# Optimization experiments

Hardware: AMD Instinct MI355X
Metric: run time of the kernel (lower is better)

Reference implementation:

```python
import jax, jax.numpy as jnp
import numpy as np

B, L, E, H = 2, 2048, 1024, 16
D = E // H
EPS = 1e-5


def setup_inputs() -> dict:
    key = jax.random.key(0)
    ks = jax.random.split(key, 12)
    s = 1.0 / np.sqrt(E)
    x = jax.random.normal(ks[0], (B, L, E), dtype=jnp.float32)
    # bool mask: True = block. Causal upper-triangular mask (L, S) with S == L.
    mask = jnp.triu(jnp.ones((L, L), dtype=jnp.bool_), k=1)
    Wq = jax.random.normal(ks[1], (E, E), jnp.float32) * s
    bq = jax.random.normal(ks[2], (E,), jnp.float32) * 0.01
    Wk = jax.random.normal(ks[3], (E, E), jnp.float32) * s
    bk = jax.random.normal(ks[4], (E,), jnp.float32) * 0.01
    Wv = jax.random.normal(ks[5], (E, E), jnp.float32) * s
    bv = jax.random.normal(ks[6], (E,), jnp.float32) * 0.01
    Wo = jax.random.normal(ks[7], (E, E), jnp.float32) * s
    bo = jax.random.normal(ks[8], (E,), jnp.float32) * 0.01
    gamma = jnp.ones((E,), jnp.float32)
    beta = jnp.zeros((E,), jnp.float32)
    return {"x": x, "mask": mask, "Wq": Wq, "bq": bq, "Wk": Wk, "bk": bk,
            "Wv": Wv, "bv": bv, "Wo": Wo, "bo": bo, "gamma": gamma, "beta": beta}


def reference(x, mask, Wq, bq, Wk, bk, Wv, bv, Wo, bo, gamma, beta):
    b, l, e = x.shape
    x = jnp.nan_to_num(x, nan=0.0, posinf=1e9, neginf=-1e9)
    # QKV projections (torch Linear: x @ W.T + b), split heads -> (B,H,L,D)
    q = (x @ Wq.T + bq).reshape(b, l, H, D).transpose(0, 2, 1, 3)
    k = (x @ Wk.T + bk).reshape(b, l, H, D).transpose(0, 2, 1, 3)
    v = (x @ Wv.T + bv).reshape(b, l, H, D).transpose(0, 2, 1, 3)
    scale = max(D ** 0.5, 1e-6)
    scores = jnp.einsum('bhtd,bhsd->bhts', q, k) / scale  # (B,H,L,L)
    # bool mask True=block -> additive -inf, broadcast (L,L) over (B,H)
    scores = scores + jnp.where(mask, -jnp.inf, 0.0).astype(scores.dtype)
    scores = scores - jnp.max(scores, axis=-1, keepdims=True)
    scores = jnp.nan_to_num(scores, nan=0.0, posinf=1e9, neginf=-1e9)
    attn = jax.nn.softmax(scores, axis=-1)
    o = jnp.einsum('bhts,bhsd->bhtd', attn, v)
    o = o.transpose(0, 2, 1, 3).reshape(b, l, e)
    y = o @ Wo.T + bo
    r = y + x
    # LayerNorm over last dim
    mu = jnp.mean(r, axis=-1, keepdims=True)
    var = jnp.mean((r - mu) ** 2, axis=-1, keepdims=True)
    out = (r - mu) * jax.lax.rsqrt(var + EPS) * gamma + beta
    out = jnp.nan_to_num(out, nan=0.0, posinf=1e9, neginf=-1e9)
    return out
```

## Files before the change

kernel.cpp:

```cpp
#include <hip/hip_runtime.h>
#include <hip/hip_bf16.h>
#include <cstdint>
#include <cstddef>

#define NB 2
#define NL 2048
#define NE 1024
#define NH 16
#define ND 64
#define NM (NB * NL)

typedef float f32x4 __attribute__((ext_vector_type(4)));
typedef __bf16 bf16x8 __attribute__((ext_vector_type(8)));
typedef __bf16 bf16x4 __attribute__((ext_vector_type(4)));

#define DEV static __device__ __forceinline__

DEV f32x4 mfma16(bf16x8 a, bf16x8 b, f32x4 c) {
  return __builtin_amdgcn_mfma_f32_16x16x32_bf16(a, b, c, 0, 0, 0);
}

DEV ushort f2bf(float f) {
  uint32_t u = __float_as_uint(f);
  uint32_t r = (u + 0x7fffu + ((u >> 16) & 1u)) >> 16;
  return (ushort)r;
}

#if __has_builtin(__builtin_amdgcn_exp2f)
DEV float fast_exp2(float x) { return __builtin_amdgcn_exp2f(x); }
#else
DEV float fast_exp2(float x) { return exp2f(x); }
#endif

DEV void gl_lds16(const void* src, void* lds_dst) {
  __builtin_amdgcn_global_load_lds(
      (const __attribute__((address_space(1))) void*)src,
      (__attribute__((address_space(3))) void*)lds_dst, 16, 0, 0);
}

template <int NCALLS>
DEV void stage_swz(const char* gbase, size_t row_stride_b, char* lds_base, int tid) {
#pragma unroll
  for (int c = 0; c < NCALLS; ++c) {
    uint32_t P = (uint32_t)(c * 4096 + tid * 16);
    uint32_t r = P >> 7;
    uint32_t Lo = P ^ ((r & 7u) << 4);
    gl_lds16(gbase + (size_t)r * row_stride_b + (Lo & 127u), lds_base + P);
  }
}

__global__ __launch_bounds__(256) void pack_kernel(
    const float* __restrict__ x, const float* __restrict__ wq,
    const float* __restrict__ wk, const float* __restrict__ wv,
    const float* __restrict__ wo, ushort* __restrict__ xb,
    ushort* __restrict__ wqb, ushort* __restrict__ wkb,
    ushort* __restrict__ wvb, ushort* __restrict__ wob) {
  int64_t q = (int64_t)blockIdx.x * 256 + threadIdx.x;
  const float* src;
  ushort* dst;
  bool cl;
  if (q < 1048576) {
    src = x + q * 4;
    dst = xb + q * 4;
    cl = true;
  } else {
    int64_t r = q - 1048576;
    int wsel = (int)(r >> 18);
    int64_t o = (r & 262143) * 4;
    cl = false;
    if (wsel == 0) { src = wq + o; dst = wqb + o; }
    else if (wsel == 1) { src = wk + o; dst = wkb + o; }
    else if (wsel == 2) { src = wv + o; dst = wvb + o; }
    else { src = wo + o; dst = wob + o; }
  }
  float4 v = *(const float4*)src;
  if (cl) {
    v.x = (v.x != v.x) ? 0.f : fminf(fmaxf(v.x, -1e9f), 1e9f);
    v.y = (v.y != v.y) ? 0.f : fminf(fmaxf(v.y, -1e9f), 1e9f);
    v.z = (v.z != v.z) ? 0.f : fminf(fmaxf(v.z, -1e9f), 1e9f);
    v.w = (v.w != v.w) ? 0.f : fminf(fmaxf(v.w, -1e9f), 1e9f);
  }
  ushort4 o4;
  o4.x = f2bf(v.x);
  o4.y = f2bf(v.y);
  o4.z = f2bf(v.z);
  o4.w = f2bf(v.w);
  *(ushort4*)dst = o4;
}

__global__ __launch_bounds__(256) void qkv_gemm_kernel(
    const ushort* __restrict__ xb, const ushort* __restrict__ wqb,
    const ushort* __restrict__ wkb, const ushort* __restrict__ wvb,
    const float* __restrict__ bq, const float* __restrict__ bk,
    const float* __restrict__ bv, ushort* __restrict__ Qo,
    ushort* __restrict__ Ko, ushort* __restrict__ Vto) {
  __shared__ __align__(128) char lds[65536];
  const int tid = threadIdx.x;
  const int w = tid >> 6, ln = tid & 63;
  const int ln15 = ln & 15, g = ln >> 4;
  const int wm = w >> 1, wn = w & 1;
  const int m0 = blockIdx.y * 128;
  const int which = blockIdx.x >> 3;
  const int n0w = (blockIdx.x & 7) * 128;
  const ushort* Wb = (which == 0) ? wqb : (which == 1) ? wkb : wvb;

  const char* Abase = (const char*)xb + (size_t)m0 * 2048;
  const char* Bbase = (const char*)Wb + (size_t)n0w * 2048;

  f32x4 acc[4][4];
#pragma unroll
  for (int m = 0; m < 4; ++m)
#pragma unroll
    for (int n = 0; n < 4; ++n) acc[m][n] = {0.f, 0.f, 0.f, 0.f};

  int cur = 0;
  stage_swz<4>(Abase, 2048, lds, tid);
  stage_swz<4>(Bbase, 2048, lds + 32768, tid);

  for (int kt = 0; kt < 16; ++kt) {
    if (kt + 1 < 16) {
      stage_swz<4>(Abase + (kt + 1) * 128, 2048, lds + (cur ^ 1) * 16384, tid);
      stage_swz<4>(Bbase + (kt + 1) * 128, 2048,
                   lds + 32768 + (cur ^ 1) * 16384, tid);
      asm volatile("s_waitcnt vmcnt(8)" ::: "memory");
    } else {
      asm volatile("s_waitcnt vmcnt(0)" ::: "memory");
    }
    __builtin_amdgcn_s_barrier();
    asm volatile("" ::: "memory");
    const char* ab = lds + cur * 16384;
    const char* bb = lds + 32768 + cur * 16384;
    __builtin_amdgcn_s_setprio(1);
#pragma unroll
    for (int kc = 0; kc < 2; ++kc) {
      bf16x8 af[4], bfr[4];
#pragma unroll
      for (int i = 0; i < 4; ++i) {
        uint32_t ar = (uint32_t)(wm * 64 + i * 16 + ln15);
        uint32_t ao = (ar * 128u + (uint32_t)(kc * 64 + g * 16)) ^ ((ar & 7u) << 4);
        af[i] = *(const bf16x8*)(ab + ao);
        uint32_t br = (uint32_t)(wn * 64 + i * 16 + ln15);
        uint32_t bo_ = (br * 128u + (uint32_t)(kc * 64 + g * 16)) ^ ((br & 7u) << 4);
        bfr[i] = *(const bf16x8*)(bb + bo_);
      }
#pragma unroll
      for (int m = 0; m < 4; ++m)
#pragma unroll
        for (int n = 0; n < 4; ++n) acc[m][n] = mfma16(af[m], bfr[n], acc[m][n]);
    }
    __builtin_amdgcn_s_setprio(0);
    asm volatile("s_waitcnt lgkmcnt(0)" ::: "memory");
    __builtin_amdgcn_s_barrier();
    asm volatile("" ::: "memory");
    cur ^= 1;
  }

  const float* bias = (which == 0) ? bq : (which == 1) ? bk : bv;
  const float sc = (which == 0) ? 0.18033688011112042f : 1.0f;
#pragma unroll
  for (int n = 0; n < 4; ++n) {
    const int col = n0w + wn * 64 + n * 16 + ln15;
    const int h = col >> 6, d = col & 63;
    const float bc = bias[col];
#pragma unroll
    for (int m = 0; m < 4; ++m) {
      if (which < 2) {
        ushort* dst = (which == 0) ? Qo : Ko;
#pragma unroll
        for (int j = 0; j < 4; ++j) {
          int mg = m0 + wm * 64 + m * 16 + g * 4 + j;
          int b = mg >> 11, l = mg & 2047;
          dst[((size_t)(b * NH + h) * NL + l) * ND + d] = f2bf((acc[m][n][j] + bc) * sc);
        }
      } else {
        int mg0 = m0 + wm * 64 + m * 16 + g * 4;
        int b = mg0 >> 11, l0 = mg0 & 2047;
        ushort4 pk;
        pk.x = f2bf(acc[m][n][0] + bc);
        pk.y = f2bf(acc[m][n][1] + bc);
        pk.z = f2bf(acc[m][n][2] + bc);
        pk.w = f2bf(acc[m][n][3] + bc);
        *(ushort4*)(Vto + ((size_t)(b * NH + h) * ND + d) * NL + l0) = pk;
      }
    }
  }
}

__global__ __launch_bounds__(256) void attn_kernel(
    const ushort* __restrict__ Q, const ushort* __restrict__ K,
    const ushort* __restrict__ Vt, ushort* __restrict__ Op) {
  __shared__ __align__(128) char lds[40960];
  const int tid = threadIdx.x;
  const int w = tid >> 6, ln = tid & 63;
  const int ln15 = ln & 15, g = ln >> 4;
  const int bx = blockIdx.x;
  const int kk = (bx >> 5) & 7, bsel = bx >> 8, bh = bx & 31;
  const int qt = (bsel == 0) ? 31 - kk : (bsel == 1) ? kk
               : (bsel == 2) ? 23 - kk : 8 + kk;
  const int b = bh >> 4, h = bh & 15;
  const ushort* Qh = Q + (size_t)bh * NL * ND;
  const ushort* Kh = K + (size_t)bh * NL * ND;
  const ushort* Vth = Vt + (size_t)bh * ND * NL;
  const uint32_t pbase = 32768u + (uint32_t)w * 2048u;

  const int qb = qt * 64;
  const int r0 = qb + w * 16;
  const int nt = qt + 1;

  bf16x8 qf[2];
#pragma unroll
  for (int kc = 0; kc < 2; ++kc)
    qf[kc] = *(const bf16x8*)(Qh + (size_t)(r0 + ln15) * ND + kc * 32 + g * 8);

  f32x4 o_acc[4];
#pragma unroll
  for (int n = 0; n < 4; ++n) o_acc[n] = {0.f, 0.f, 0.f, 0.f};
  float m_run = -1e30f, l_run = 0.f;

  int cur = 0;
  stage_swz<2>((const char*)Kh, 128, lds, tid);
  stage_swz<2>((const char*)Vth, (size_t)NL * 2, lds + 16384, tid);

  for (int t = 0; t < nt; ++t) {
    const int s0 = t * 64;
    if (t + 1 < nt) {
      stage_swz<2>((const char*)Kh + (size_t)(s0 + 64) * 128, 128,
                   lds + (cur ^ 1) * 8192, tid);
      stage_swz<2>((const char*)Vth + (size_t)(s0 + 64) * 2, (size_t)NL * 2,
                   lds + 16384 + (cur ^ 1) * 8192, tid);
      asm volatile("s_waitcnt vmcnt(4)" ::: "memory");
    } else {
      asm volatile("s_waitcnt vmcnt(0)" ::: "memory");
    }
    __builtin_amdgcn_s_barrier();
    asm volatile("" ::: "memory");

    const char* kb = lds + cur * 8192;
    const char* vb = lds + 16384 + cur * 8192;

    f32x4 s_acc[4];
#pragma unroll
    for (int n = 0; n < 4; ++n) s_acc[n] = {0.f, 0.f, 0.f, 0.f};
    __builtin_amdgcn_s_setprio(1);
#pragma unroll
    for (int kc = 0; kc < 2; ++kc) {
      bf16x8 kf[4];
#pragma unroll
      for (int n = 0; n < 4; ++n) {
        uint32_t kr = (uint32_t)(n * 16 + ln15);
        uint32_t off = (kr * 128u + (uint32_t)(kc * 64 + g * 16)) ^ ((kr & 7u) << 4);
        kf[n] = *(const bf16x8*)(kb + off);
      }
#pragma unroll
      for (int n = 0; n < 4; ++n) s_acc[n] = mfma16(kf[n], qf[kc], s_acc[n]);
    }
    __builtin_amdgcn_s_setprio(0);

    if (t == nt - 1) {
      const int qi = r0 + ln15;
#pragma unroll
      for (int n = 0; n < 4; ++n)
#pragma unroll
        for (int j = 0; j < 4; ++j) {
          int si = s0 + n * 16 + g * 4 + j;
          s_acc[n][j] = (si > qi) ? -1e30f : s_acc[n][j];
        }
    }

    float mx = s_acc[0][0];
#pragma unroll
    for (int n = 0; n < 4; ++n)
#pragma unroll
      for (int j = 0; j < 4; ++j) mx = fmaxf(mx, s_acc[n][j]);
    mx = fmaxf(mx, __shfl_xor(mx, 16));
    mx = fmaxf(mx, __shfl_xor(mx, 32));
    if (__any(mx > m_run + 8.0f)) {
      float mn = fmaxf(m_run, mx);
      float al = fast_exp2(m_run - mn);
      m_run = mn;
      l_run *= al;
#pragma unroll
      for (int j = 0; j < 4; ++j) {
        float aj = __shfl(al, g * 4 + j);
#pragma unroll
        for (int n = 0; n < 4; ++n) o_acc[n][j] *= aj;
      }
    }
    float ps = 0.f;
#pragma unroll
    for (int n = 0; n < 4; ++n) {
      float p0 = fast_exp2(s_acc[n][0] - m_run);
      float p1 = fast_exp2(s_acc[n][1] - m_run);
      float p2 = fast_exp2(s_acc[n][2] - m_run);
      float p3 = fast_exp2(s_acc[n][3] - m_run);
      ps += (p0 + p1) + (p2 + p3);
      bf16x4 pk = {(__bf16)p0, (__bf16)p1, (__bf16)p2, (__bf16)p3};
      uint32_t off = ((uint32_t)ln15 * 128u + (uint32_t)(n * 32 + g * 8)) ^
                     (((uint32_t)ln15 & 7u) << 4);
      *(bf16x4*)(lds + pbase + off) = pk;
    }
    ps += __shfl_xor(ps, 16);
    ps += __shfl_xor(ps, 32);
    l_run += ps;

    __builtin_amdgcn_s_setprio(1);
#pragma unroll
    for (int kc = 0; kc < 2; ++kc) {
      uint32_t poff = ((uint32_t)ln15 * 128u + (uint32_t)(kc * 64 + g * 16)) ^
                      (((uint32_t)ln15 & 7u) << 4);
      bf16x8 pf = *(const bf16x8*)(lds + pbase + poff);
      bf16x8 vf[4];
#pragma unroll
      for (int n = 0; n < 4; ++n) {
        uint32_t vr = (uint32_t)(n * 16 + ln15);
        uint32_t off = (vr * 128u + (uint32_t)(kc * 64 + g * 16)) ^ ((vr & 7u) << 4);
        vf[n] = *(const bf16x8*)(vb + off);
      }
#pragma unroll
      for (int n = 0; n < 4; ++n) o_acc[n] = mfma16(pf, vf[n], o_acc[n]);
    }
    __builtin_amdgcn_s_setprio(0);

    asm volatile("s_waitcnt lgkmcnt(0)" ::: "memory");
    __builtin_amdgcn_s_barrier();
    asm volatile("" ::: "memory");
    cur ^= 1;
  }

  float invl = 1.0f / l_run;
#pragma unroll
  for (int j = 0; j < 4; ++j) {
    float inv = __shfl(invl, g * 4 + j);
    int qi = r0 + g * 4 + j;
    size_t rowo = ((size_t)b * NL + qi) * NE + h * ND;
#pragma unroll
    for (int n = 0; n < 4; ++n) Op[rowo + n * 16 + ln15] = f2bf(o_acc[n][j] * inv);
  }
}

__global__ __launch_bounds__(256) void oproj_kernel(
    const ushort* __restrict__ ob, const ushort* __restrict__ wob,
    const float* __restrict__ bo, const float* __restrict__ x,
    float* __restrict__ out) {
  __shared__ __align__(128) char lds[65536];
  const int tid = threadIdx.x;
  const int w = tid >> 6, ln = tid & 63;
  const int ln15 = ln & 15, g = ln >> 4;
  const int wm = w >> 1, wn = w & 1;
  const int m0 = blockIdx.y * 128;
  const int n0 = blockIdx.x * 128;

  const char* Abase = (const char*)ob + (size_t)m0 * 2048;
  const char* Bbase = (const char*)wob + (size_t)n0 * 2048;

  f32x4 acc[4][4];
#pragma unroll
  for (int m = 0; m < 4; ++m)
#pragma unroll
    for (int n = 0; n < 4; ++n) acc[m][n] = {0.f, 0.f, 0.f, 0.f};

  int cur = 0;
  stage_swz<4>(Abase, 2048, lds, tid);
  stage_swz<4>(Bbase, 2048, lds + 32768, tid);

  for (int kt = 0; kt < 16; ++kt) {
    if (kt + 1 < 16) {
      stage_swz<4>(Abase + (kt + 1) * 128, 2048, lds + (cur ^ 1) * 16384, tid);
      stage_swz<4>(Bbase + (kt + 1) * 128, 2048,
                   lds + 32768 + (cur ^ 1) * 16384, tid);
      asm volatile("s_waitcnt vmcnt(8)" ::: "memory");
    } else {
      asm volatile("s_waitcnt vmcnt(0)" ::: "memory");
    }
    __builtin_amdgcn_s_barrier();
    asm volatile("" ::: "memory");
    const char* ab = lds + cur * 16384;
    const char* bb = lds + 32768 + cur * 16384;
    __builtin_amdgcn_s_setprio(1);
#pragma unroll
    for (int kc = 0; kc < 2; ++kc) {
      bf16x8 af[4], bfr[4];
#pragma unroll
      for (int i = 0; i < 4; ++i) {
        uint32_t ar = (uint32_t)(wm * 64 + i * 16 + ln15);
        uint32_t ao = (ar * 128u + (uint32_t)(kc * 64 + g * 16)) ^ ((ar & 7u) << 4);
        af[i] = *(const bf16x8*)(ab + ao);
        uint32_t br = (uint32_t)(wn * 64 + i * 16 + ln15);
        uint32_t bo_ = (br * 128u + (uint32_t)(kc * 64 + g * 16)) ^ ((br & 7u) << 4);
        bfr[i] = *(const bf16x8*)(bb + bo_);
      }
#pragma unroll
      for (int m = 0; m < 4; ++m)
#pragma unroll
        for (int n = 0; n < 4; ++n) acc[m][n] = mfma16(af[m], bfr[n], acc[m][n]);
    }
    __builtin_amdgcn_s_setprio(0);
    asm volatile("s_waitcnt lgkmcnt(0)" ::: "memory");
    __builtin_amdgcn_s_barrier();
    asm volatile("" ::: "memory");
    cur ^= 1;
  }

#pragma unroll
  for (int n = 0; n < 4; ++n) {
    const int col = n0 + wn * 64 + n * 16 + ln15;
    const float bc = bo[col];
#pragma unroll
    for (int m = 0; m < 4; ++m)
#pragma unroll
      for (int j = 0; j < 4; ++j) {
        int mg = m0 + wm * 64 + m * 16 + g * 4 + j;
        size_t idx = (size_t)mg * NE + col;
        out[idx] = acc[m][n][j] + bc + x[idx];
      }
  }
}

__global__ __launch_bounds__(256) void ln_kernel(float* __restrict__ io,
                                                 const float* __restrict__ gamma,
                                                 const float* __restrict__ beta) {
  const int row = blockIdx.x, tid = threadIdx.x;
  const int w = tid >> 6, ln = tid & 63;
  float4 v = *(const float4*)(io + (size_t)row * NE + tid * 4);
  float s = v.x + v.y + v.z + v.w;
  float ss = v.x * v.x + v.y * v.y + v.z * v.z + v.w * v.w;
#pragma unroll
  for (int d = 1; d < 64; d <<= 1) {
    s += __shfl_xor(s, d);
    ss += __shfl_xor(ss, d);
  }
  __shared__ float red[8];
  if (ln == 0) {
    red[w] = s;
    red[4 + w] = ss;
  }
  __syncthreads();
  s = red[0] + red[1] + red[2] + red[3];
  ss = red[4] + red[5] + red[6] + red[7];
  const float mu = s * (1.0f / (float)NE);
  float var = ss * (1.0f / (float)NE) - mu * mu;
  const float inv = rsqrtf(var + 1e-5f);
  float4 gv = *(const float4*)(gamma + tid * 4);
  float4 bv = *(const float4*)(beta + tid * 4);
  float4 o;
  o.x = (v.x - mu) * inv * gv.x + bv.x;
  o.y = (v.y - mu) * inv * gv.y + bv.y;
  o.z = (v.z - mu) * inv * gv.z + bv.z;
  o.w = (v.w - mu) * inv * gv.w + bv.w;
  *(float4*)(io + (size_t)row * NE + tid * 4) = o;
}

extern "C" void kernel_launch(void* const* d_in, const int* in_sizes, int n_in,
                              void* d_out, int out_size, void* d_ws, size_t ws_size,
                              hipStream_t stream) {
  const float* x = (const float*)d_in[0];
  const float* Wq = (const float*)d_in[2];
  const float* bq = (const float*)d_in[3];
  const float* Wk = (const float*)d_in[4];
  const float* bk = (const float*)d_in[5];
  const float* Wv = (const float*)d_in[6];
  const float* bv = (const float*)d_in[7];
  const float* Wo = (const float*)d_in[8];
  const float* bo = (const float*)d_in[9];
  const float* gamma = (const float*)d_in[10];
  const float* beta = (const float*)d_in[11];

  char* ws = (char*)d_ws;
  ushort* xb  = (ushort*)(ws + 0);
  ushort* wqb = (ushort*)(ws + 8388608);
  ushort* wkb = (ushort*)(ws + 10485760);
  ushort* wvb = (ushort*)(ws + 12582912);
  ushort* wob = (ushort*)(ws + 14680064);
  ushort* Qb  = (ushort*)(ws + 16777216);
  ushort* Kb  = (ushort*)(ws + 25165824);
  ushort* Vtb = (ushort*)(ws + 33554432);
  ushort* Ob  = (ushort*)(ws + 41943040);

  pack_kernel<<<8192, 256, 0, stream>>>(x, Wq, Wk, Wv, Wo, xb, wqb, wkb, wvb, wob);
  qkv_gemm_kernel<<<dim3(24, 32), 256, 0, stream>>>(xb, wqb, wkb, wvb, bq, bk, bv,
                                                    Qb, Kb, Vtb);
  attn_kernel<<<1024, 256, 0, stream>>>(Qb, Kb, Vtb, Ob);
  oproj_kernel<<<dim3(8, 32), 256, 0, stream>>>(Ob, wob, bo, x, (float*)d_out);
  ln_kernel<<<4096, 256, 0, stream>>>((float*)d_out, gamma, beta);
}
```

Before: 114.5 us.

## Restructure attention into single-wave blocks loading K/V directly into registers

Each attention block becomes one 64-lane wave that handles 32 query rows with two sets of accumulators. K and V tiles are read from global memory straight into registers, with a two-stage software prefetch, instead of being staged through shared memory. This removes the LDS staging and the block barriers. The P@V MFMA operand order is swapped so the output can be stored as packed ushort4 rows, and the grid uses 2048 blocks ordered from the longest causal tiles first. In exchange, each wave fetches its own copy of K/V from global/L2, so memory traffic and register pressure go up.

New measurement: 137.7 us. 1.2x slower.

```diff
diff --git a/kernel.cpp b/kernel.cpp
--- a/kernel.cpp
+++ b/kernel.cpp
@@ -186,155 +186,151 @@
   }
 }
 
-__global__ __launch_bounds__(256) void attn_kernel(
+#define ISSUE_K(DST, t_)                                                      \
+  do {                                                                        \
+    const int s_ = (t_) * 64;                                                 \
+    _Pragma("unroll") for (int kc = 0; kc < 2; ++kc)                          \
+        _Pragma("unroll") for (int n = 0; n < 4; ++n)                         \
+            DST[kc][n] = *(const bf16x8*)(Kh +                                \
+                (size_t)(s_ + n * 16 + ln15) * ND + kc * 32 + g * 8);         \
+  } while (0)
+
+#define ISSUE_V(t_)                                                           \
+  do {                                                                        \
+    const int s_ = (t_) * 64;                                                 \
+    _Pragma("unroll") for (int kc = 0; kc < 2; ++kc)                          \
+        _Pragma("unroll") for (int n = 0; n < 4; ++n)                         \
+            vf[kc][n] = *(const bf16x8*)(Vth +                                \
+                (size_t)(n * 16 + ln15) * NL + s_ + kc * 32 + g * 8);         \
+  } while (0)
+
+#define COMPUTE(KF, t_)                                                       \
+  do {                                                                        \
+    const int s0 = (t_) * 64;                                                 \
+    f32x4 s_acc[2][4];                                                        \
+    _Pragma("unroll") for (int m = 0; m < 2; ++m)                             \
+        _Pragma("unroll") for (int n = 0; n < 4; ++n)                         \
+            s_acc[m][n] = {0.f, 0.f, 0.f, 0.f};                               \
+    __builtin_amdgcn_s_setprio(1);                                            \
+    _Pragma("unroll") for (int kc = 0; kc < 2; ++kc)                          \
+        _Pragma("unroll") for (int n = 0; n < 4; ++n)                         \
+            _Pragma("unroll") for (int m = 0; m < 2; ++m)                     \
+                s_acc[m][n] = mfma16(KF[kc][n], qf[m][kc], s_acc[m][n]);      \
+    __builtin_amdgcn_s_setprio(0);                                            \
+    if (s0 + 63 > q0) {                   \
+      _Pragma("unroll") for (int m = 0; m < 2; ++m) {                         \
+        const int qi = q0 + m * 16 + ln15;                                    \
+        _Pragma("unroll") for (int n = 0; n < 4; ++n)                         \
+            _Pragma("unroll") for (int j = 0; j < 4; ++j) {                   \
+              int si = s0 + n * 16 + g * 4 + j;                               \
+              s_acc[m][n][j] = (si > qi) ? -1e30f : s_acc[m][n][j];           \
+            }                                                                 \
+      }                                                                       \
+    }                                                                         \
+    _Pragma("unroll") for (int m = 0; m < 2; ++m) {                           \
+      float mx = s_acc[m][0][0];                                              \
+      _Pragma("unroll") for (int n = 0; n < 4; ++n)                           \
+          _Pragma("unroll") for (int j = 0; j < 4; ++j)                       \
+              mx = fmaxf(mx, s_acc[m][n][j]);                                 \
+      mx = fmaxf(mx, __shfl_xor(mx, 16));                                     \
+      mx = fmaxf(mx, __shfl_xor(mx, 32));                                     \
+      if (__any(mx > m_run[m] + 8.0f)) {             \
+        float mn = fmaxf(m_run[m], mx);                                       \
+        float al = fast_exp2(m_run[m] - mn);                                  \
+        m_run[m] = mn;                                                        \
+        l_run[m] *= al;                                                       \
+        _Pragma("unroll") for (int n = 0; n < 4; ++n)                         \
+            _Pragma("unroll") for (int j = 0; j < 4; ++j)                     \
+                o_acc[m][n][j] *= al;            \
+      }                                                                       \
+      float ps = 0.f;                                                         \
+      _Pragma("unroll") for (int n = 0; n < 4; ++n) {                         \
+        float p0 = fast_exp2(s_acc[m][n][0] - m_run[m]);                      \
+        float p1 = fast_exp2(s_acc[m][n][1] - m_run[m]);                      \
+        float p2 = fast_exp2(s_acc[m][n][2] - m_run[m]);                      \
+        float p3 = fast_exp2(s_acc[m][n][3] - m_run[m]);                      \
+        ps += (p0 + p1) + (p2 + p3);                                          \
+        bf16x4 pk = {(__bf16)p0, (__bf16)p1, (__bf16)p2, (__bf16)p3};         \
+        uint32_t off = ((uint32_t)ln15 * 128u +                               \
+                        (uint32_t)(n * 32 + g * 8)) ^                         \
+                       (((uint32_t)ln15 & 7u) << 4);                          \
+        *(bf16x4*)(lds + m * 2048 + off) = pk;                                \
+      }                                                                       \
+      ps += __shfl_xor(ps, 16);                                               \
+      ps += __shfl_xor(ps, 32);                                               \
+      l_run[m] += ps;                                                         \
+    }                                                                         \
+    __builtin_amdgcn_s_setprio(1);                                            \
+    _Pragma("unroll") for (int m = 0; m < 2; ++m)                             \
+        _Pragma("unroll") for (int kc = 0; kc < 2; ++kc) {                    \
+          uint32_t poff = ((uint32_t)ln15 * 128u +                            \
+                           (uint32_t)(kc * 64 + g * 16)) ^                    \
+                          (((uint32_t)ln15 & 7u) << 4);                       \
+          bf16x8 pf = *(const bf16x8*)(lds + m * 2048 + poff);                \
+          _Pragma("unroll") for (int n = 0; n < 4; ++n)                       \
+              o_acc[m][n] = mfma16(vf[kc][n], pf, o_acc[m][n]);               \
+        }                                                                     \
+    __builtin_amdgcn_s_setprio(0);                                            \
+  } while (0)
+
+__global__ __launch_bounds__(64) void attn_kernel(
     const ushort* __restrict__ Q, const ushort* __restrict__ K,
     const ushort* __restrict__ Vt, ushort* __restrict__ Op) {
-  __shared__ __align__(128) char lds[40960];
-  const int tid = threadIdx.x;
-  const int w = tid >> 6, ln = tid & 63;
+  __shared__ __align__(128) char lds[4096];
+  const int ln = threadIdx.x;
   const int ln15 = ln & 15, g = ln >> 4;
   const int bx = blockIdx.x;
-  const int kk = (bx >> 5) & 7, bsel = bx >> 8, bh = bx & 31;
-  const int qt = (bsel == 0) ? 31 - kk : (bsel == 1) ? kk
-               : (bsel == 2) ? 23 - kk : 8 + kk;
+  const int bh = bx & 31;
+  const int tt = bx >> 5;
+  const int qt = 63 - tt;
+  const int q0 = qt * 32;
   const int b = bh >> 4, h = bh & 15;
   const ushort* Qh = Q + (size_t)bh * NL * ND;
   const ushort* Kh = K + (size_t)bh * NL * ND;
   const ushort* Vth = Vt + (size_t)bh * ND * NL;
-  const uint32_t pbase = 32768u + (uint32_t)w * 2048u;
-
-  const int qb = qt * 64;
-  const int r0 = qb + w * 16;
-  const int nt = qt + 1;
-
-  bf16x8 qf[2];
-#pragma unroll
-  for (int kc = 0; kc < 2; ++kc)
-    qf[kc] = *(const bf16x8*)(Qh + (size_t)(r0 + ln15) * ND + kc * 32 + g * 8);
-
-  f32x4 o_acc[4];
-#pragma unroll
-  for (int n = 0; n < 4; ++n) o_acc[n] = {0.f, 0.f, 0.f, 0.f};
-  float m_run = -1e30f, l_run = 0.f;
-
-  int cur = 0;
-  stage_swz<2>((const char*)Kh, 128, lds, tid);
-  stage_swz<2>((const char*)Vth, (size_t)NL * 2, lds + 16384, tid);
-
-  for (int t = 0; t < nt; ++t) {
-    const int s0 = t * 64;
-    if (t + 1 < nt) {
-      stage_swz<2>((const char*)Kh + (size_t)(s0 + 64) * 128, 128,
-                   lds + (cur ^ 1) * 8192, tid);
-      stage_swz<2>((const char*)Vth + (size_t)(s0 + 64) * 2, (size_t)NL * 2,
-                   lds + 16384 + (cur ^ 1) * 8192, tid);
-      asm volatile("s_waitcnt vmcnt(4)" ::: "memory");
-    } else {
-      asm volatile("s_waitcnt vmcnt(0)" ::: "memory");
-    }
-    __builtin_amdgcn_s_barrier();
-    asm volatile("" ::: "memory");
-
-    const char* kb = lds + cur * 8192;
-    const char* vb = lds + 16384 + cur * 8192;
-
-    f32x4 s_acc[4];
-#pragma unroll
-    for (int n = 0; n < 4; ++n) s_acc[n] = {0.f, 0.f, 0.f, 0.f};
-    __builtin_amdgcn_s_setprio(1);
-#pragma unroll
-    for (int kc = 0; kc < 2; ++kc) {
-      bf16x8 kf[4];
-#pragma unroll
-      for (int n = 0; n < 4; ++n) {
-        uint32_t kr = (uint32_t)(n * 16 + ln15);
-        uint32_t off = (kr * 128u + (uint32_t)(kc * 64 + g * 16)) ^ ((kr & 7u) << 4);
-        kf[n] = *(const bf16x8*)(kb + off);
-      }
-#pragma unroll
-      for (int n = 0; n < 4; ++n) s_acc[n] = mfma16(kf[n], qf[kc], s_acc[n]);
-    }
-    __builtin_amdgcn_s_setprio(0);
-
-    if (t == nt - 1) {
-      const int qi = r0 + ln15;
-#pragma unroll
-      for (int n = 0; n < 4; ++n)
-#pragma unroll
-        for (int j = 0; j < 4; ++j) {
-          int si = s0 + n * 16 + g * 4 + j;
-          s_acc[n][j] = (si > qi) ? -1e30f : s_acc[n][j];
-        }
-    }
-
-    float mx = s_acc[0][0];
-#pragma unroll
-    for (int n = 0; n < 4; ++n)
-#pragma unroll
-      for (int j = 0; j < 4; ++j) mx = fmaxf(mx, s_acc[n][j]);
-    mx = fmaxf(mx, __shfl_xor(mx, 16));
-    mx = fmaxf(mx, __shfl_xor(mx, 32));
-    if (__any(mx > m_run + 8.0f)) {
-      float mn = fmaxf(m_run, mx);
-      float al = fast_exp2(m_run - mn);
-      m_run = mn;
-      l_run *= al;
-#pragma unroll
-      for (int j = 0; j < 4; ++j) {
-        float aj = __shfl(al, g * 4 + j);
-#pragma unroll
-        for (int n = 0; n < 4; ++n) o_acc[n][j] *= aj;
-      }
-    }
-    float ps = 0.f;
+  const int nt = qt / 2 + 1;
+  const int nt_e = (nt + 1) & ~1;
+
+  bf16x8 qf[2][2];
+#pragma unroll
+  for (int m = 0; m < 2; ++m)
+#pragma unroll
+    for (int kc = 0; kc < 2; ++kc)
+      qf[m][kc] = *(const bf16x8*)(Qh + (size_t)(q0 + m * 16 + ln15) * ND +
+                                   kc * 32 + g * 8);
+
+  f32x4 o_acc[2][4];
+#pragma unroll
+  for (int m = 0; m < 2; ++m)
+#pragma unroll
+    for (int n = 0; n < 4; ++n) o_acc[m][n] = {0.f, 0.f, 0.f, 0.f};
+  float m_run[2] = {-1e30f, -1e30f}, l_run[2] = {0.f, 0.f};
+
+  bf16x8 kfA[2][4], kfB[2][4], vf[2][4];
+  ISSUE_K(kfA, 0);
+
+  for (int t = 0; t < nt_e; t += 2) {
+    ISSUE_V(t);
+    ISSUE_K(kfB, t + 1);
+    COMPUTE(kfA, t);
+    ISSUE_V(t + 1);
+    if (t + 2 < nt_e) ISSUE_K(kfA, t + 2);
+    COMPUTE(kfB, t + 1);
+  }
+
+#pragma unroll
+  for (int m = 0; m < 2; ++m) {
+    float inv = 1.0f / l_run[m];
+    size_t rowo = ((size_t)(b * NL + q0 + m * 16 + ln15)) * NE + h * ND;
 #pragma unroll
     for (int n = 0; n < 4; ++n) {
-      float p0 = fast_exp2(s_acc[n][0] - m_run);
-      float p1 = fast_exp2(s_acc[n][1] - m_run);
-      float p2 = fast_exp2(s_acc[n][2] - m_run);
-      float p3 = fast_exp2(s_acc[n][3] - m_run);
-      ps += (p0 + p1) + (p2 + p3);
-      bf16x4 pk = {(__bf16)p0, (__bf16)p1, (__bf16)p2, (__bf16)p3};
-      uint32_t off = ((uint32_t)ln15 * 128u + (uint32_t)(n * 32 + g * 8)) ^
-                     (((uint32_t)ln15 & 7u) << 4);
-      *(bf16x4*)(lds + pbase + off) = pk;
-    }
-    ps += __shfl_xor(ps, 16);
-    ps += __shfl_xor(ps, 32);
-    l_run += ps;
-
-    __builtin_amdgcn_s_setprio(1);
-#pragma unroll
-    for (int kc = 0; kc < 2; ++kc) {
-      uint32_t poff = ((uint32_t)ln15 * 128u + (uint32_t)(kc * 64 + g * 16)) ^
-                      (((uint32_t)ln15 & 7u) << 4);
-      bf16x8 pf = *(const bf16x8*)(lds + pbase + poff);
-      bf16x8 vf[4];
-#pragma unroll
-      for (int n = 0; n < 4; ++n) {
-        uint32_t vr = (uint32_t)(n * 16 + ln15);
-        uint32_t off = (vr * 128u + (uint32_t)(kc * 64 + g * 16)) ^ ((vr & 7u) << 4);
-        vf[n] = *(const bf16x8*)(vb + off);
-      }
-#pragma unroll
-      for (int n = 0; n < 4; ++n) o_acc[n] = mfma16(pf, vf[n], o_acc[n]);
-    }
-    __builtin_amdgcn_s_setprio(0);
-
-    asm volatile("s_waitcnt lgkmcnt(0)" ::: "memory");
-    __builtin_amdgcn_s_barrier();
-    asm volatile("" ::: "memory");
-    cur ^= 1;
-  }
-
-  float invl = 1.0f / l_run;
-#pragma unroll
-  for (int j = 0; j < 4; ++j) {
-    float inv = __shfl(invl, g * 4 + j);
-    int qi = r0 + g * 4 + j;
-    size_t rowo = ((size_t)b * NL + qi) * NE + h * ND;
-#pragma unroll
-    for (int n = 0; n < 4; ++n) Op[rowo + n * 16 + ln15] = f2bf(o_acc[n][j] * inv);
+      ushort4 st;
+      st.x = f2bf(o_acc[m][n][0] * inv);
+      st.y = f2bf(o_acc[m][n][1] * inv);
+      st.z = f2bf(o_acc[m][n][2] * inv);
+      st.w = f2bf(o_acc[m][n][3] * inv);
+      *(ushort4*)(Op + rowo + n * 16 + g * 4) = st;
+    }
   }
 }
 
@@ -479,7 +475,7 @@
   pack_kernel<<<8192, 256, 0, stream>>>(x, Wq, Wk, Wv, Wo, xb, wqb, wkb, wvb, wob);
   qkv_gemm_kernel<<<dim3(24, 32), 256, 0, stream>>>(xb, wqb, wkb, wvb, bq, bk, bv,
                                                     Qb, Kb, Vtb);
-  attn_kernel<<<1024, 256, 0, stream>>>(Qb, Kb, Vtb, Ob);
+  attn_kernel<<<2048, 64, 0, stream>>>(Qb, Kb, Vtb, Ob);
   oproj_kernel<<<dim3(8, 32), 256, 0, stream>>>(Ob, wob, bo, x, (float*)d_out);
   ln_kernel<<<4096, 256, 0, stream>>>((float*)d_out, gamma, beta);
 }
```

## Split long causal attention rows across two KV chunks with a combine kernel

Applied to the files above, without the earlier changes.

Query tiles whose causal range exceeds 16 KV tiles are now processed by two blocks, each covering up to 16 KV tiles. Each block writes unnormalized bf16 partial outputs plus its running max and sum to scratch workspace reused from the packed-x and Wq regions. A new combine kernel merges the two partials with log-sum-exp weights. This shortens the longest per-block critical path and improves load balance across CUs. The cost is an extra launch, extra global traffic for partials, and blocks that exit immediately because they have no KV range.

New measurement: 113.1 us. About the same (-1.2%).

```diff
diff --git a/kernel.cpp b/kernel.cpp
--- a/kernel.cpp
+++ b/kernel.cpp
@@ -25,6 +25,8 @@
   uint32_t r = (u + 0x7fffu + ((u >> 16) & 1u)) >> 16;
   return (ushort)r;
 }
+
+DEV float bf2f(ushort u) { return __uint_as_float((uint32_t)u << 16); }
 
 #if __has_builtin(__builtin_amdgcn_exp2f)
 DEV float fast_exp2(float x) { return __builtin_amdgcn_exp2f(x); }
@@ -188,24 +190,29 @@
 
 __global__ __launch_bounds__(256) void attn_kernel(
     const ushort* __restrict__ Q, const ushort* __restrict__ K,
-    const ushort* __restrict__ Vt, ushort* __restrict__ Op) {
+    const ushort* __restrict__ Vt, ushort* __restrict__ Op,
+    ushort* __restrict__ po, float* __restrict__ pml) {
   __shared__ __align__(128) char lds[40960];
   const int tid = threadIdx.x;
   const int w = tid >> 6, ln = tid & 63;
   const int ln15 = ln & 15, g = ln >> 4;
   const int bx = blockIdx.x;
-  const int kk = (bx >> 5) & 7, bsel = bx >> 8, bh = bx & 31;
-  const int qt = (bsel == 0) ? 31 - kk : (bsel == 1) ? kk
-               : (bsel == 2) ? 23 - kk : 8 + kk;
+  const int qt = 31 - (bx >> 6);
+  const int ci = (bx >> 5) & 1;
+  const int bh = bx & 31;
+  const int nt = qt + 1;
+  const int lo = ci * 16;
+  const int hi = (nt < lo + 16) ? nt : lo + 16;
+  if (hi <= lo) return;
+
   const int b = bh >> 4, h = bh & 15;
   const ushort* Qh = Q + (size_t)bh * NL * ND;
   const ushort* Kh = K + (size_t)bh * NL * ND;
   const ushort* Vth = Vt + (size_t)bh * ND * NL;
   const uint32_t pbase = 32768u + (uint32_t)w * 2048u;
 
-  const int qb = qt * 64;
-  const int r0 = qb + w * 16;
-  const int nt = qt + 1;
+  const int q0 = qt * 64;
+  const int r0 = q0 + w * 16;
 
   bf16x8 qf[2];
 #pragma unroll
@@ -218,12 +225,12 @@
   float m_run = -1e30f, l_run = 0.f;
 
   int cur = 0;
-  stage_swz<2>((const char*)Kh, 128, lds, tid);
-  stage_swz<2>((const char*)Vth, (size_t)NL * 2, lds + 16384, tid);
-
-  for (int t = 0; t < nt; ++t) {
+  stage_swz<2>((const char*)Kh + (size_t)lo * 64 * 128, 128, lds, tid);
+  stage_swz<2>((const char*)Vth + (size_t)lo * 64 * 2, (size_t)NL * 2, lds + 16384, tid);
+
+  for (int t = lo; t < hi; ++t) {
     const int s0 = t * 64;
-    if (t + 1 < nt) {
+    if (t + 1 < hi) {
       stage_swz<2>((const char*)Kh + (size_t)(s0 + 64) * 128, 128,
                    lds + (cur ^ 1) * 8192, tid);
       stage_swz<2>((const char*)Vth + (size_t)(s0 + 64) * 2, (size_t)NL * 2,
@@ -327,15 +334,69 @@
     cur ^= 1;
   }
 
-  float invl = 1.0f / l_run;
-#pragma unroll
-  for (int j = 0; j < 4; ++j) {
-    float inv = __shfl(invl, g * 4 + j);
-    int qi = r0 + g * 4 + j;
-    size_t rowo = ((size_t)b * NL + qi) * NE + h * ND;
-#pragma unroll
-    for (int n = 0; n < 4; ++n) Op[rowo + n * 16 + ln15] = f2bf(o_acc[n][j] * inv);
-  }
+  if (nt <= 16) {
+    float invl = 1.0f / l_run;
+#pragma unroll
+    for (int j = 0; j < 4; ++j) {
+      float inv = __shfl(invl, g * 4 + j);
+      int qi = r0 + g * 4 + j;
+      size_t rowo = ((size_t)b * NL + qi) * NE + h * ND;
+#pragma unroll
+      for (int n = 0; n < 4; ++n) Op[rowo + n * 16 + ln15] = f2bf(o_acc[n][j] * inv);
+    }
+  } else {
+    const int slot = (bh * 16 + (qt - 16)) * 2 + ci;
+    ushort* so = po + (size_t)slot * 4096;
+#pragma unroll
+    for (int j = 0; j < 4; ++j) {
+      int ql = w * 16 + g * 4 + j;
+#pragma unroll
+      for (int n = 0; n < 4; ++n) so[ql * 64 + n * 16 + ln15] = f2bf(o_acc[n][j]);
+    }
+    if (g == 0) {
+      pml[(size_t)slot * 128 + (w * 16 + ln15) * 2] = m_run;
+      pml[(size_t)slot * 128 + (w * 16 + ln15) * 2 + 1] = l_run;
+    }
+  }
+}
+
+__global__ __launch_bounds__(256) void attn_combine_kernel(
+    const ushort* __restrict__ po, const float* __restrict__ pml,
+    ushort* __restrict__ Op) {
+  const int bx = blockIdx.x;
+  const int qt = 16 + (bx >> 5), bh = bx & 31;
+  const int b = bh >> 4, h = bh & 15;
+  const int tid = threadIdx.x;
+  const int row = tid >> 2, dseg = (tid & 3) * 16;
+  const int slot = (bh * 16 + (qt - 16)) * 2;
+  const float* ml1 = pml + (size_t)slot * 128 + row * 2;
+  const float* ml2 = pml + (size_t)(slot + 1) * 128 + row * 2;
+  const float m1 = ml1[0], l1 = ml1[1];
+  const float m2 = ml2[0], l2 = ml2[1];
+  const float M = fmaxf(m1, m2);
+  const float w1 = fast_exp2(m1 - M), w2 = fast_exp2(m2 - M);
+  const float inv = 1.0f / (w1 * l1 + w2 * l2);
+  const ushort* o1 = po + (size_t)slot * 4096 + row * 64 + dseg;
+  const ushort* o2 = po + (size_t)(slot + 1) * 4096 + row * 64 + dseg;
+  ushort4 r1a = *(const ushort4*)o1, r1b = *(const ushort4*)(o1 + 4);
+  ushort4 r1c = *(const ushort4*)(o1 + 8), r1d = *(const ushort4*)(o1 + 12);
+  ushort4 r2a = *(const ushort4*)o2, r2b = *(const ushort4*)(o2 + 4);
+  ushort4 r2c = *(const ushort4*)(o2 + 8), r2d = *(const ushort4*)(o2 + 12);
+  ushort out[16];
+  const ushort* p1 = &r1a.x;
+  const ushort* p2 = &r2a.x;
+  ushort q1[16] = {r1a.x, r1a.y, r1a.z, r1a.w, r1b.x, r1b.y, r1b.z, r1b.w,
+                   r1c.x, r1c.y, r1c.z, r1c.w, r1d.x, r1d.y, r1d.z, r1d.w};
+  ushort q2[16] = {r2a.x, r2a.y, r2a.z, r2a.w, r2b.x, r2b.y, r2b.z, r2b.w,
+                   r2c.x, r2c.y, r2c.z, r2c.w, r2d.x, r2d.y, r2d.z, r2d.w};
+  (void)p1; (void)p2;
+#pragma unroll
+  for (int i = 0; i < 16; ++i)
+    out[i] = f2bf((w1 * bf2f(q1[i]) + w2 * bf2f(q2[i])) * inv);
+  ushort* dst = Op + ((size_t)(b * NL + qt * 64 + row)) * NE + h * ND + dseg;
+#pragma unroll
+  for (int i = 0; i < 4; ++i)
+    *(ushort4*)(dst + i * 4) = *(ushort4*)(out + i * 4);
 }
 
 __global__ __launch_bounds__(256) void oproj_kernel(
@@ -475,11 +536,14 @@
   ushort* Kb  = (ushort*)(ws + 25165824);
   ushort* Vtb = (ushort*)(ws + 33554432);
   ushort* Ob  = (ushort*)(ws + 41943040);
+  ushort* po  = (ushort*)(ws + 0);
+  float*  pml = (float*)(ws + 8388608);
 
   pack_kernel<<<8192, 256, 0, stream>>>(x, Wq, Wk, Wv, Wo, xb, wqb, wkb, wvb, wob);
   qkv_gemm_kernel<<<dim3(24, 32), 256, 0, stream>>>(xb, wqb, wkb, wvb, bq, bk, bv,
                                                     Qb, Kb, Vtb);
-  attn_kernel<<<1024, 256, 0, stream>>>(Qb, Kb, Vtb, Ob);
+  attn_kernel<<<2048, 256, 0, stream>>>(Qb, Kb, Vtb, Ob, po, pml);
+  attn_combine_kernel<<<512, 256, 0, stream>>>(po, pml, Ob);
   oproj_kernel<<<dim3(8, 32), 256, 0, stream>>>(Ob, wob, bo, x, (float*)d_out);
   ln_kernel<<<4096, 256, 0, stream>>>((float*)d_out, gamma, beta);
 }
```

## Use one barrier per K-step and 128-row, 512-thread attention blocks

Applied to the files above, without the earlier changes.

In both GEMM kernels and the attention kernel the double-buffered loop now uses a single wait-and-barrier at the top of each step instead of two barriers, and the next tile's prefetch is issued only after that barrier. The attention kernel moves to 512-thread blocks covering 128 query rows with 8 waves that share each K/V tile. Waves skip tiles that lie entirely above the causal diagonal, and the row-sum reduction across lanes is deferred to the end. The intent is fewer barriers and less K/V staging per query row. The cost is that loads no longer overlap the preceding wait, and waves with less causal work sit idle, which is a load imbalance.

New measurement: 105.7 us (median of 2 runs). 7.7% less time.

```diff
diff --git a/kernel.cpp b/kernel.cpp
--- a/kernel.cpp
+++ b/kernel.cpp
@@ -47,6 +47,13 @@
     uint32_t Lo = P ^ ((r & 7u) << 4);
     gl_lds16(gbase + (size_t)r * row_stride_b + (Lo & 127u), lds_base + P);
   }
+}
+
+DEV void stage8k_swz(const char* gbase, size_t row_stride_b, char* lds_base, int tid) {
+  uint32_t P = (uint32_t)(tid * 16);
+  uint32_t r = P >> 7;
+  uint32_t Lo = P ^ ((r & 7u) << 4);
+  gl_lds16(gbase + (size_t)r * row_stride_b + (Lo & 127u), lds_base + P);
 }
 
 __global__ __launch_bounds__(256) void pack_kernel(
@@ -118,16 +125,14 @@
   stage_swz<4>(Bbase, 2048, lds + 32768, tid);
 
   for (int kt = 0; kt < 16; ++kt) {
+    asm volatile("s_waitcnt vmcnt(0)" ::: "memory");
+    __builtin_amdgcn_s_barrier();
+    asm volatile("" ::: "memory");
     if (kt + 1 < 16) {
       stage_swz<4>(Abase + (kt + 1) * 128, 2048, lds + (cur ^ 1) * 16384, tid);
       stage_swz<4>(Bbase + (kt + 1) * 128, 2048,
                    lds + 32768 + (cur ^ 1) * 16384, tid);
-      asm volatile("s_waitcnt vmcnt(8)" ::: "memory");
-    } else {
-      asm volatile("s_waitcnt vmcnt(0)" ::: "memory");
-    }
-    __builtin_amdgcn_s_barrier();
-    asm volatile("" ::: "memory");
+    }
     const char* ab = lds + cur * 16384;
     const char* bb = lds + 32768 + cur * 16384;
     __builtin_amdgcn_s_setprio(1);
@@ -149,9 +154,6 @@
         for (int n = 0; n < 4; ++n) acc[m][n] = mfma16(af[m], bfr[n], acc[m][n]);
     }
     __builtin_amdgcn_s_setprio(0);
-    asm volatile("s_waitcnt lgkmcnt(0)" ::: "memory");
-    __builtin_amdgcn_s_barrier();
-    asm volatile("" ::: "memory");
     cur ^= 1;
   }
 
@@ -186,26 +188,27 @@
   }
 }
 
-__global__ __launch_bounds__(256) void attn_kernel(
+__global__ __launch_bounds__(512) void attn_kernel(
     const ushort* __restrict__ Q, const ushort* __restrict__ K,
     const ushort* __restrict__ Vt, ushort* __restrict__ Op) {
-  __shared__ __align__(128) char lds[40960];
+  __shared__ __align__(128) char lds[49152];
   const int tid = threadIdx.x;
   const int w = tid >> 6, ln = tid & 63;
   const int ln15 = ln & 15, g = ln >> 4;
   const int bx = blockIdx.x;
-  const int kk = (bx >> 5) & 7, bsel = bx >> 8, bh = bx & 31;
-  const int qt = (bsel == 0) ? 31 - kk : (bsel == 1) ? kk
-               : (bsel == 2) ? 23 - kk : 8 + kk;
+  const int bh = bx & 31;
+  const int seg = bx >> 5;
+  const int qt = (seg < 8) ? 15 - seg : seg - 8;
+  const int nt = 2 * qt + 2;
+
   const int b = bh >> 4, h = bh & 15;
   const ushort* Qh = Q + (size_t)bh * NL * ND;
   const ushort* Kh = K + (size_t)bh * NL * ND;
   const ushort* Vth = Vt + (size_t)bh * ND * NL;
   const uint32_t pbase = 32768u + (uint32_t)w * 2048u;
 
-  const int qb = qt * 64;
-  const int r0 = qb + w * 16;
-  const int nt = qt + 1;
+  const int q0 = qt * 128;
+  const int r0 = q0 + w * 16;
 
   bf16x8 qf[2];
 #pragma unroll
@@ -218,114 +221,117 @@
   float m_run = -1e30f, l_run = 0.f;
 
   int cur = 0;
-  stage_swz<2>((const char*)Kh, 128, lds, tid);
-  stage_swz<2>((const char*)Vth, (size_t)NL * 2, lds + 16384, tid);
+  stage8k_swz((const char*)Kh, 128, lds, tid);
+  stage8k_swz((const char*)Vth, (size_t)NL * 2, lds + 16384, tid);
 
   for (int t = 0; t < nt; ++t) {
     const int s0 = t * 64;
-    if (t + 1 < nt) {
-      stage_swz<2>((const char*)Kh + (size_t)(s0 + 64) * 128, 128,
-                   lds + (cur ^ 1) * 8192, tid);
-      stage_swz<2>((const char*)Vth + (size_t)(s0 + 64) * 2, (size_t)NL * 2,
-                   lds + 16384 + (cur ^ 1) * 8192, tid);
-      asm volatile("s_waitcnt vmcnt(4)" ::: "memory");
-    } else {
-      asm volatile("s_waitcnt vmcnt(0)" ::: "memory");
-    }
+    asm volatile("s_waitcnt vmcnt(0)" ::: "memory");
     __builtin_amdgcn_s_barrier();
     asm volatile("" ::: "memory");
-
-    const char* kb = lds + cur * 8192;
-    const char* vb = lds + 16384 + cur * 8192;
-
-    f32x4 s_acc[4];
-#pragma unroll
-    for (int n = 0; n < 4; ++n) s_acc[n] = {0.f, 0.f, 0.f, 0.f};
-    __builtin_amdgcn_s_setprio(1);
-#pragma unroll
-    for (int kc = 0; kc < 2; ++kc) {
-      bf16x8 kf[4];
+    if (t + 1 < nt) {
+      stage8k_swz((const char*)Kh + (size_t)(s0 + 64) * 128, 128,
+                  lds + (cur ^ 1) * 8192, tid);
+      stage8k_swz((const char*)Vth + (size_t)(s0 + 64) * 2, (size_t)NL * 2,
+                  lds + 16384 + (cur ^ 1) * 8192, tid);
+    }
+
+    if (s0 <= r0 + 15) {
+      const char* kb = lds + cur * 8192;
+      const char* vb = lds + 16384 + cur * 8192;
+
+      f32x4 s_acc[4];
+#pragma unroll
+      for (int n = 0; n < 4; ++n) s_acc[n] = {0.f, 0.f, 0.f, 0.f};
+      __builtin_amdgcn_s_setprio(1);
+#pragma unroll
+      for (int kc = 0; kc < 2; ++kc) {
+        bf16x8 kf[4];
+#pragma unroll
+        for (int n = 0; n < 4; ++n) {
+          uint32_t kr = (uint32_t)(n * 16 + ln15);
+          uint32_t off = (kr * 128u + (uint32_t)(kc * 64 + g * 16)) ^ ((kr & 7u) << 4);
+          kf[n] = *(const bf16x8*)(kb + off);
+        }
+#pragma unroll
+        for (int n = 0; n < 4; ++n) s_acc[n] = mfma16(kf[n], qf[kc], s_acc[n]);
+      }
+      __builtin_amdgcn_s_setprio(0);
+
+      if (s0 + 63 > r0) {
+        const int qi = r0 + ln15;
+#pragma unroll
+        for (int n = 0; n < 4; ++n)
+#pragma unroll
+          for (int j = 0; j < 4; ++j) {
+            int si = s0 + n * 16 + g * 4 + j;
+            s_acc[n][j] = (si > qi) ? -1e30f : s_acc[n][j];
+          }
+      }
+
+      float mx;
+      {
+        float a0 = fmaxf(fmaxf(s_acc[0][0], s_acc[0][1]), s_acc[0][2]);
+        float a1 = fmaxf(fmaxf(s_acc[0][3], s_acc[1][0]), s_acc[1][1]);
+        float a2 = fmaxf(fmaxf(s_acc[1][2], s_acc[1][3]), s_acc[2][0]);
+        float a3 = fmaxf(fmaxf(s_acc[2][1], s_acc[2][2]), s_acc[2][3]);
+        float a4 = fmaxf(fmaxf(s_acc[3][0], s_acc[3][1]), s_acc[3][2]);
+        float b0 = fmaxf(fmaxf(a0, a1), a2);
+        float b1 = fmaxf(fmaxf(a3, a4), s_acc[3][3]);
+        mx = fmaxf(b0, b1);
+      }
+      if (__any(mx > m_run + 8.0f)) {
+        float mr = fmaxf(mx, __shfl_xor(mx, 16));
+        mr = fmaxf(mr, __shfl_xor(mr, 32));
+        float mn = fmaxf(m_run, mr);
+        float al = fast_exp2(m_run - mn);
+        m_run = mn;
+        l_run *= al;
+#pragma unroll
+        for (int j = 0; j < 4; ++j) {
+          float aj = __shfl(al, g * 4 + j);
+#pragma unroll
+          for (int n = 0; n < 4; ++n) o_acc[n][j] *= aj;
+        }
+      }
+      float ps = 0.f;
 #pragma unroll
       for (int n = 0; n < 4; ++n) {
-        uint32_t kr = (uint32_t)(n * 16 + ln15);
-        uint32_t off = (kr * 128u + (uint32_t)(kc * 64 + g * 16)) ^ ((kr & 7u) << 4);
-        kf[n] = *(const bf16x8*)(kb + off);
-      }
-#pragma unroll
-      for (int n = 0; n < 4; ++n) s_acc[n] = mfma16(kf[n], qf[kc], s_acc[n]);
-    }
-    __builtin_amdgcn_s_setprio(0);
-
-    if (t == nt - 1) {
-      const int qi = r0 + ln15;
-#pragma unroll
-      for (int n = 0; n < 4; ++n)
-#pragma unroll
-        for (int j = 0; j < 4; ++j) {
-          int si = s0 + n * 16 + g * 4 + j;
-          s_acc[n][j] = (si > qi) ? -1e30f : s_acc[n][j];
+        float p0 = fast_exp2(s_acc[n][0] - m_run);
+        float p1 = fast_exp2(s_acc[n][1] - m_run);
+        float p2 = fast_exp2(s_acc[n][2] - m_run);
+        float p3 = fast_exp2(s_acc[n][3] - m_run);
+        ps += (p0 + p1) + (p2 + p3);
+        bf16x4 pk = {(__bf16)p0, (__bf16)p1, (__bf16)p2, (__bf16)p3};
+        uint32_t off = ((uint32_t)ln15 * 128u + (uint32_t)(n * 32 + g * 8)) ^
+                       (((uint32_t)ln15 & 7u) << 4);
+        *(bf16x4*)(lds + pbase + off) = pk;
+      }
+      l_run += ps;
+
+      __builtin_amdgcn_s_setprio(1);
+#pragma unroll
+      for (int kc = 0; kc < 2; ++kc) {
+        uint32_t poff = ((uint32_t)ln15 * 128u + (uint32_t)(kc * 64 + g * 16)) ^
+                        (((uint32_t)ln15 & 7u) << 4);
+        bf16x8 pf = *(const bf16x8*)(lds + pbase + poff);
+        bf16x8 vf[4];
+#pragma unroll
+        for (int n = 0; n < 4; ++n) {
+          uint32_t vr = (uint32_t)(n * 16 + ln15);
+          uint32_t off = (vr * 128u + (uint32_t)(kc * 64 + g * 16)) ^ ((vr & 7u) << 4);
+          vf[n] = *(const bf16x8*)(vb + off);
         }
-    }
-
-    float mx = s_acc[0][0];
-#pragma unroll
-    for (int n = 0; n < 4; ++n)
-#pragma unroll
-      for (int j = 0; j < 4; ++j) mx = fmaxf(mx, s_acc[n][j]);
-    mx = fmaxf(mx, __shfl_xor(mx, 16));
-    mx = fmaxf(mx, __shfl_xor(mx, 32));
-    if (__any(mx > m_run + 8.0f)) {
-      float mn = fmaxf(m_run, mx);
-      float al = fast_exp2(m_run - mn);
-      m_run = mn;
-      l_run *= al;
-#pragma unroll
-      for (int j = 0; j < 4; ++j) {
-        float aj = __shfl(al, g * 4 + j);
-#pragma unroll
-        for (int n = 0; n < 4; ++n) o_acc[n][j] *= aj;
-      }
-    }
-    float ps = 0.f;
-#pragma unroll
-    for (int n = 0; n < 4; ++n) {
-      float p0 = fast_exp2(s_acc[n][0] - m_run);
-      float p1 = fast_exp2(s_acc[n][1] - m_run);
-      float p2 = fast_exp2(s_acc[n][2] - m_run);
-      float p3 = fast_exp2(s_acc[n][3] - m_run);
-      ps += (p0 + p1) + (p2 + p3);
-      bf16x4 pk = {(__bf16)p0, (__bf16)p1, (__bf16)p2, (__bf16)p3};
-      uint32_t off = ((uint32_t)ln15 * 128u + (uint32_t)(n * 32 + g * 8)) ^
-                     (((uint32_t)ln15 & 7u) << 4);
-      *(bf16x4*)(lds + pbase + off) = pk;
-    }
-    ps += __shfl_xor(ps, 16);
-    ps += __shfl_xor(ps, 32);
-    l_run += ps;
-
-    __builtin_amdgcn_s_setprio(1);
-#pragma unroll
-    for (int kc = 0; kc < 2; ++kc) {
-      uint32_t poff = ((uint32_t)ln15 * 128u + (uint32_t)(kc * 64 + g * 16)) ^
-                      (((uint32_t)ln15 & 7u) << 4);
-      bf16x8 pf = *(const bf16x8*)(lds + pbase + poff);
-      bf16x8 vf[4];
-#pragma unroll
-      for (int n = 0; n < 4; ++n) {
-        uint32_t vr = (uint32_t)(n * 16 + ln15);
-        uint32_t off = (vr * 128u + (uint32_t)(kc * 64 + g * 16)) ^ ((vr & 7u) << 4);
-        vf[n] = *(const bf16x8*)(vb + off);
-      }
-#pragma unroll
-      for (int n = 0; n < 4; ++n) o_acc[n] = mfma16(pf, vf[n], o_acc[n]);
-    }
-    __builtin_amdgcn_s_setprio(0);
-
-    asm volatile("s_waitcnt lgkmcnt(0)" ::: "memory");
-    __builtin_amdgcn_s_barrier();
-    asm volatile("" ::: "memory");
+#pragma unroll
+        for (int n = 0; n < 4; ++n) o_acc[n] = mfma16(pf, vf[n], o_acc[n]);
+      }
+      __builtin_amdgcn_s_setprio(0);
+    }
     cur ^= 1;
   }
+
+  l_run += __shfl_xor(l_run, 16);
+  l_run += __shfl_xor(l_run, 32);
 
   float invl = 1.0f / l_run;
 #pragma unroll
@@ -364,16 +370,14 @@
   stage_swz<4>(Bbase, 2048, lds + 32768, tid);
 
   for (int kt = 0; kt < 16; ++kt) {
+    asm volatile("s_waitcnt vmcnt(0)" ::: "memory");
+    __builtin_amdgcn_s_barrier();
+    asm volatile("" ::: "memory");
     if (kt + 1 < 16) {
       stage_swz<4>(Abase + (kt + 1) * 128, 2048, lds + (cur ^ 1) * 16384, tid);
       stage_swz<4>(Bbase + (kt + 1) * 128, 2048,
                    lds + 32768 + (cur ^ 1) * 16384, tid);
-      asm volatile("s_waitcnt vmcnt(8)" ::: "memory");
-    } else {
-      asm volatile("s_waitcnt vmcnt(0)" ::: "memory");
-    }
-    __builtin_amdgcn_s_barrier();
-    asm volatile("" ::: "memory");
+    }
     const char* ab = lds + cur * 16384;
     const char* bb = lds + 32768 + cur * 16384;
     __builtin_amdgcn_s_setprio(1);
@@ -395,9 +399,6 @@
         for (int n = 0; n < 4; ++n) acc[m][n] = mfma16(af[m], bfr[n], acc[m][n]);
     }
     __builtin_amdgcn_s_setprio(0);
-    asm volatile("s_waitcnt lgkmcnt(0)" ::: "memory");
-    __builtin_amdgcn_s_barrier();
-    asm volatile("" ::: "memory");
     cur ^= 1;
   }
 
@@ -479,7 +480,7 @@
   pack_kernel<<<8192, 256, 0, stream>>>(x, Wq, Wk, Wv, Wo, xb, wqb, wkb, wvb, wob);
   qkv_gemm_kernel<<<dim3(24, 32), 256, 0, stream>>>(xb, wqb, wkb, wvb, bq, bk, bv,
                                                     Qb, Kb, Vtb);
-  attn_kernel<<<1024, 256, 0, stream>>>(Qb, Kb, Vtb, Ob);
+  attn_kernel<<<512, 512, 0, stream>>>(Qb, Kb, Vtb, Ob);
   oproj_kernel<<<dim3(8, 32), 256, 0, stream>>>(Ob, wob, bo, x, (float*)d_out);
   ln_kernel<<<4096, 256, 0, stream>>>((float*)d_out, gamma, beta);
 }
```
